# Performance work log

Hardware: AMD Instinct MI355X
Metric: run time of the kernel (lower is better)

## Reference

```python
import jax, jax.numpy as jnp
import numpy as np

NP, NC, E, EL = 50000, 5000, 200000, 100000
DP, DC, HID, OUT, HEADS = 1280, 256, 128, 128, 4


def setup_inputs() -> dict:
    key = jax.random.key(0)
    ks = jax.random.split(key, 40)
    p = lambda k, shp: jax.random.normal(k, shp, dtype=jnp.float32) * 0.05
    inp = {
        "x_protein": jax.random.normal(ks[0], (NP, DP), dtype=jnp.float32),
        "x_class": jax.random.normal(ks[1], (NC, DC), dtype=jnp.float32),
        "src": jax.random.randint(ks[2], (E,), 0, NP),
        "dst": jax.random.randint(ks[3], (E,), 0, NC),
        "edge_label_src": jax.random.randint(ks[4], (EL,), 0, NP),
        "edge_label_dst": jax.random.randint(ks[5], (EL,), 0, NC),
        # SAGEConv, relation protein->class (updates class nodes)
        "sage_pc_Wl": p(ks[6], (DP, HID)), "sage_pc_bl": p(ks[7], (HID,)), "sage_pc_Wr": p(ks[8], (DC, HID)),
        # SAGEConv, relation class->protein (updates protein nodes)
        "sage_cp_Wl": p(ks[9], (DC, HID)), "sage_cp_bl": p(ks[10], (HID,)), "sage_cp_Wr": p(ks[11], (DP, HID)),
        # GATConv p->c (inputs are hidden after conv1)
        "gat_pc_Wsrc": p(ks[12], (HID, HEADS * HID)), "gat_pc_Wdst": p(ks[13], (HID, HEADS * HID)),
        "gat_pc_asrc": p(ks[14], (HEADS, HID)), "gat_pc_adst": p(ks[15], (HEADS, HID)), "gat_pc_b": p(ks[16], (HID,)),
        # GATConv c->p
        "gat_cp_Wsrc": p(ks[17], (HID, HEADS * HID)), "gat_cp_Wdst": p(ks[18], (HID, HEADS * HID)),
        "gat_cp_asrc": p(ks[19], (HEADS, HID)), "gat_cp_adst": p(ks[20], (HEADS, HID)), "gat_cp_b": p(ks[21], (HID,)),
        # final per-node-type Linear (to_hetero duplicates lin per node type)
        "lin_p_W": p(ks[22], (HID, OUT)), "lin_p_b": p(ks[23], (OUT,)),
        "lin_c_W": p(ks[24], (HID, OUT)), "lin_c_b": p(ks[25], (OUT,)),
        # link predictor
        "link_W": p(ks[26], (2 * OUT, 1)), "link_b": p(ks[27], (1,)),
    }
    return inp


def _sage(x_src, x_dst, s, d, Wl, bl, Wr, n_dst):
    # PyG SAGEConv: lin_l(mean_aggr(x_src)) + lin_r(x_dst); lin_l has bias.
    agg = jax.ops.segment_sum(x_src[s], d, num_segments=n_dst)
    cnt = jax.ops.segment_sum(jnp.ones((s.shape[0], 1), x_src.dtype), d, num_segments=n_dst)
    mean = agg / jnp.maximum(cnt, 1.0)
    return mean @ Wl + bl + x_dst @ Wr


def _gat(x_src, x_dst, s, d, Ws, Wd, a_s, a_d, b, n_dst):
    # PyG GATConv bipartite, heads=HEADS, concat=False, add_self_loops=False.
    H, C = a_s.shape
    hs = (x_src @ Ws).reshape(-1, H, C)   # [Ns, H, C]
    hd = (x_dst @ Wd).reshape(-1, H, C)   # [Nd, H, C]
    als = jnp.einsum('nhc,hc->nh', hs, a_s)
    ald = jnp.einsum('nhc,hc->nh', hd, a_d)
    e = jax.nn.leaky_relu(als[s] + ald[d], 0.2)                    # [E, H]
    emax = jax.ops.segment_max(e, d, num_segments=n_dst)          # stable softmax per dst
    ee = jnp.exp(e - emax[d])
    denom = jax.ops.segment_sum(ee, d, num_segments=n_dst)
    alpha = ee / denom[d]                                          # [E, H]
    out = jax.ops.segment_sum(alpha[:, :, None] * hs[s], d, num_segments=n_dst)  # [Nd, H, C]
    return out.mean(axis=1) + b  # concat=False -> mean over heads


def reference(x_protein, x_class, src, dst, edge_label_src, edge_label_dst,
              sage_pc_Wl, sage_pc_bl, sage_pc_Wr,
              sage_cp_Wl, sage_cp_bl, sage_cp_Wr,
              gat_pc_Wsrc, gat_pc_Wdst, gat_pc_asrc, gat_pc_adst, gat_pc_b,
              gat_cp_Wsrc, gat_cp_Wdst, gat_cp_asrc, gat_cp_adst, gat_cp_b,
              lin_p_W, lin_p_b, lin_c_W, lin_c_b, link_W, link_b):
    # Layer 1: hetero SAGE (each node type has exactly one incoming relation)
    h_c = jax.nn.relu(_sage(x_protein, x_class, src, dst, sage_pc_Wl, sage_pc_bl, sage_pc_Wr, NC))
    h_p = jax.nn.relu(_sage(x_class, x_protein, dst, src, sage_cp_Wl, sage_cp_bl, sage_cp_Wr, NP))
    # Layer 2: hetero GAT
    g_c = jax.nn.relu(_gat(h_p, h_c, src, dst, gat_pc_Wsrc, gat_pc_Wdst, gat_pc_asrc, gat_pc_adst, gat_pc_b, NC))
    g_p = jax.nn.relu(_gat(h_c, h_p, dst, src, gat_cp_Wsrc, gat_cp_Wdst, gat_cp_asrc, gat_cp_adst, gat_cp_b, NP))
    # Per-type output projection
    z_p = g_p @ lin_p_W + lin_p_b
    z_c = g_c @ lin_c_W + lin_c_b
    # Link predictor: gather, concat, linear, sigmoid
    ef = jnp.concatenate([z_p[edge_label_src], z_c[edge_label_dst]], axis=-1)  # [EL, 2*OUT]
    return jax.nn.sigmoid(ef @ link_W + link_b).squeeze(-1)
```

## Files before the change

kernel.cpp:

```cpp
#include <hip/hip_runtime.h>
#include <math.h>

#define NPROT 50000
#define NCLS  5000
#define DIMP  1280
#define DIMC  256
#define SCAN_N (NCLS + NPROT)

typedef float4 f4;
typedef __attribute__((ext_vector_type(8))) short short8;
typedef __attribute__((ext_vector_type(4))) float f32x4;

__device__ __forceinline__ unsigned short f2bf(float f){
    unsigned u = __float_as_uint(f);
    u += 0x7FFFu + ((u >> 16) & 1u);
    return (unsigned short)(u >> 16);
}
__device__ __forceinline__ float bf2f(unsigned short b){
    return __uint_as_float(((unsigned)b) << 16);
}
__device__ __forceinline__ void gload_lds16(const void* g, void* l){
    __builtin_amdgcn_global_load_lds((const __attribute__((address_space(1))) void*)g,
                                     (__attribute__((address_space(3))) void*)l, 16, 0, 0);
}

__global__ __launch_bounds__(512) void gemm_p1(const float* __restrict__ Af,
                                               const unsigned short* __restrict__ Bt,
                                               unsigned short* __restrict__ C, int M){
    __shared__ __align__(16) unsigned char As[128*32*4];
    __shared__ __align__(16) unsigned char Bs[256*32*2];
    const int tid  = threadIdx.x;
    const int lane = tid & 63;
    const int w    = tid >> 6;
    const int wm   = w >> 2, wn = w & 3;
    const int row0 = blockIdx.x * 128;
    const int kg = lane >> 4, fr = lane & 15;

    f32x4 acc[4][4] = {};

    for(int k0 = 0; k0 < DIMP; k0 += 32){
        #pragma unroll
        for(int i=0;i<2;i++){
            int c  = i*512 + w*64 + lane;
            int r  = c >> 3, cc = c & 7;
            int scc = cc ^ (r & 7);
            int srow = min(row0 + r, M-1);
            gload_lds16((const void*)(Af + (size_t)srow*DIMP + k0 + scc*4),
                        (void*)(As + (i*512 + w*64)*16));
        }
        #pragma unroll
        for(int i=0;i<2;i++){
            int c  = i*512 + w*64 + lane;
            int r  = c >> 2, cc = c & 3;
            int scc = cc ^ ((r>>1) & 3);
            gload_lds16((const void*)(Bt + (size_t)r*DIMP + k0 + scc*8),
                        (void*)(Bs + (i*512 + w*64)*16));
        }
        __syncthreads();

        short8 aF[4], bF[4];
        #pragma unroll
        for(int m=0;m<4;m++){
            int r = wm*64 + m*16 + fr;
            int b0 = r*128 + kg*32;
            f4 lo = *(const f4*)(As + (( b0      ) ^ ((r&7)<<4)));
            f4 hi = *(const f4*)(As + (( b0 + 16 ) ^ ((r&7)<<4)));
            union { short8 s; unsigned short u[8]; } uu;
            uu.u[0]=f2bf(lo.x); uu.u[1]=f2bf(lo.y); uu.u[2]=f2bf(lo.z); uu.u[3]=f2bf(lo.w);
            uu.u[4]=f2bf(hi.x); uu.u[5]=f2bf(hi.y); uu.u[6]=f2bf(hi.z); uu.u[7]=f2bf(hi.w);
            aF[m] = uu.s;
        }
        #pragma unroll
        for(int n=0;n<4;n++){
            int r = wn*64 + n*16 + fr;
            int b0 = (r*64 + kg*16) ^ (((r>>1)&3)<<4);
            bF[n] = *(const short8*)(Bs + b0);
        }
        #pragma unroll
        for(int m=0;m<4;m++)
        #pragma unroll
        for(int n=0;n<4;n++)
            acc[m][n] = __builtin_amdgcn_mfma_f32_16x16x32_bf16(aF[m], bF[n], acc[m][n], 0, 0, 0);
        __syncthreads();
    }

    #pragma unroll
    for(int m=0;m<4;m++)
    #pragma unroll
    for(int r=0;r<4;r++){
        int row = row0 + wm*64 + m*16 + kg*4 + r;
        if(row < M){
            #pragma unroll
            for(int n=0;n<4;n++)
                C[(size_t)row*256 + wn*64 + n*16 + fr] = f2bf(acc[m][n][r]);
        }
    }
}

#define NPB ((NPROT+127)/128)
#define NCB ((NCLS+127)/128)
__global__ __launch_bounds__(256) void gemm_hs(const unsigned short* __restrict__ Ap,
                                               const unsigned short* __restrict__ Ac,
                                               const unsigned short* __restrict__ Btp,
                                               const unsigned short* __restrict__ Btc,
                                               unsigned short* __restrict__ Cp,
                                               unsigned short* __restrict__ Cc){
    const bool cls = (int)blockIdx.y >= NPB;
    const unsigned short* A  = cls ? Ac : Ap;
    const unsigned short* Bt = cls ? Btc : Btp;
    unsigned short* C = cls ? Cc : Cp;
    const int M = cls ? NCLS : NPROT;
    const int row0 = (cls ? blockIdx.y - NPB : blockIdx.y) * 128;
    const int col0 = blockIdx.x * 128;

    __shared__ __align__(16) unsigned char As[128*32*2];
    __shared__ __align__(16) unsigned char Bs[128*32*2];
    const int tid  = threadIdx.x;
    const int lane = tid & 63;
    const int w    = tid >> 6;
    const int wm   = w >> 1, wn = w & 1;
    const int kg = lane >> 4, fr = lane & 15;

    f32x4 acc[4][4] = {};

    for(int k0 = 0; k0 < 128; k0 += 32){
        #pragma unroll
        for(int i=0;i<2;i++){
            int c  = i*256 + w*64 + lane;
            int r  = c >> 2, cc = c & 3;
            int scc = cc ^ ((r>>1) & 3);
            int srow = min(row0 + r, M-1);
            gload_lds16((const void*)(A + (size_t)srow*128 + k0 + scc*8),
                        (void*)(As + (i*256 + w*64)*16));
        }
        #pragma unroll
        for(int i=0;i<2;i++){
            int c  = i*256 + w*64 + lane;
            int r  = c >> 2, cc = c & 3;
            int scc = cc ^ ((r>>1) & 3);
            gload_lds16((const void*)(Bt + (size_t)(col0 + r)*128 + k0 + scc*8),
                        (void*)(Bs + (i*256 + w*64)*16));
        }
        __syncthreads();

        short8 aF[4], bF[4];
        #pragma unroll
        for(int m=0;m<4;m++){
            int r = wm*64 + m*16 + fr;
            int b0 = (r*64 + kg*16) ^ (((r>>1)&3)<<4);
            aF[m] = *(const short8*)(As + b0);
        }
        #pragma unroll
        for(int n=0;n<4;n++){
            int r = wn*64 + n*16 + fr;
            int b0 = (r*64 + kg*16) ^ (((r>>1)&3)<<4);
            bF[n] = *(const short8*)(Bs + b0);
        }
        #pragma unroll
        for(int m=0;m<4;m++)
        #pragma unroll
        for(int n=0;n<4;n++)
            acc[m][n] = __builtin_amdgcn_mfma_f32_16x16x32_bf16(aF[m], bF[n], acc[m][n], 0, 0, 0);
        __syncthreads();
    }

    #pragma unroll
    for(int m=0;m<4;m++)
    #pragma unroll
    for(int r=0;r<4;r++){
        int row = row0 + wm*64 + m*16 + kg*4 + r;
        if(row < M){
            #pragma unroll
            for(int n=0;n<4;n++)
                C[(size_t)row*512 + col0 + wn*64 + n*16 + fr] = f2bf(acc[m][n][r]);
        }
    }
}

__global__ __launch_bounds__(256) void gemm64(const float* __restrict__ A,
                                              const float* __restrict__ B,
                                              float* __restrict__ C,
                                              int M, int N, int K){
    __shared__ __align__(16) float As[16][68];
    __shared__ __align__(16) float Bs[16][64];
    const int tid = threadIdx.x;
    const int row0 = blockIdx.y * 64;
    const int col0 = blockIdx.x * 64;
    const int ty = tid >> 4;
    const int tx = tid & 15;
    const int m  = tid >> 2;
    const int kq = (tid & 3) << 2;
    const int kb = tid >> 4;
    const int c4 = (tid & 15) << 2;

    float acc[4][4];
#pragma unroll
    for(int i=0;i<4;i++)
#pragma unroll
        for(int j=0;j<4;j++) acc[i][j]=0.f;

    const bool arow_ok = (row0 + m) < M;
    const float* Abase = A + (size_t)(row0 + m) * K + kq;
    const float* Bbase = B + col0 + c4 + (size_t)kb * N;

    for(int k0 = 0; k0 < K; k0 += 16){
        f4 av;
        if(arow_ok) av = *(const f4*)(Abase + k0);
        else        av = make_float4(0.f,0.f,0.f,0.f);
        As[kq+0][m]=av.x; As[kq+1][m]=av.y; As[kq+2][m]=av.z; As[kq+3][m]=av.w;
        *(f4*)&Bs[kb][c4] = *(const f4*)(Bbase + (size_t)k0 * N);
        __syncthreads();
#pragma unroll
        for(int kk=0;kk<16;kk++){
            f4 a = *(const f4*)&As[kk][ty<<2];
            f4 b = *(const f4*)&Bs[kk][tx<<2];
            float ar[4]={a.x,a.y,a.z,a.w};
            float br[4]={b.x,b.y,b.z,b.w};
#pragma unroll
            for(int i=0;i<4;i++)
#pragma unroll
                for(int j=0;j<4;j++) acc[i][j] += ar[i]*br[j];
        }
        __syncthreads();
    }
#pragma unroll
    for(int i=0;i<4;i++){
        int r = row0 + (ty<<2) + i;
        if(r < M){
            f4 v = make_float4(acc[i][0],acc[i][1],acc[i][2],acc[i][3]);
            *(f4*)&C[(size_t)r*N + col0 + (tx<<2)] = v;
        }
    }
}

__global__ __launch_bounds__(256) void gemm_n8_all(const unsigned short* __restrict__ h_p,
                                                   const unsigned short* __restrict__ h_c,
                                                   const float* __restrict__ projP,
                                                   const float* __restrict__ projC,
                                                   float* __restrict__ attP,
                                                   float* __restrict__ attC){
    __shared__ float Bs[2048];
    const int tid = threadIdx.x;
    for(int i=tid;i<1024;i+=256){ Bs[i]=projP[i]; Bs[1024+i]=projC[i]; }
    __syncthreads();
    const int row = blockIdx.x*32 + (tid>>3);
    const int j = tid & 7;
    if(row >= NPROT+NCLS) return;
    const bool cls = row >= NPROT;
    const int r = cls ? row - NPROT : row;
    const unsigned short* a = (cls ? h_c : h_p) + (size_t)r*128;
    const float* B = Bs + (cls ? 1024 : 0);
    float s=0.f;
#pragma unroll
    for(int k=0;k<128;k++) s += bf2f(a[k])*B[k*8+j];
    (cls ? attC : attP)[(size_t)r*8+j]=s;
}

__global__ void prep_weights(const float* __restrict__ Wl_pc, const float* __restrict__ Wr_cp,
                             const float* __restrict__ Wl_cp, const float* __restrict__ Wr_pc,
                             const float* __restrict__ Ws_pc, const float* __restrict__ Ws_cp,
                             unsigned short* __restrict__ BtP, float* __restrict__ WcatC,
                             unsigned short* __restrict__ BtSp, unsigned short* __restrict__ BtSc){
    int t = blockIdx.x*256 + threadIdx.x;
    if(t < 327680){
        int n = t / 1280, k = t % 1280;
        float v = (n<128) ? Wl_pc[(size_t)k*128+n] : Wr_cp[(size_t)k*128+n-128];
        BtP[t] = f2bf(v);
    } else if(t < 393216){
        int i = t - 327680; int k = i>>8, j = i&255;
        WcatC[i] = (j<128) ? Wl_cp[(size_t)k*128+j] : Wr_pc[(size_t)k*128+j-128];
    } else if(t < 458752){
        int i = t - 393216; int n = i>>7, k = i&127;
        BtSp[i] = f2bf(Ws_pc[(size_t)k*512+n]);
    } else {
        int i = t - 458752; int n = i>>7, k = i&127;
        BtSc[i] = f2bf(Ws_cp[(size_t)k*512+n]);
    }
}

__global__ void folds(const float* __restrict__ pcWs, const float* __restrict__ pcAs,
                      const float* __restrict__ pcWd, const float* __restrict__ pcAd,
                      const float* __restrict__ cpWs, const float* __restrict__ cpAs,
                      const float* __restrict__ cpWd, const float* __restrict__ cpAd,
                      const float* __restrict__ lpW, const float* __restrict__ lpb,
                      const float* __restrict__ lcW, const float* __restrict__ lcb,
                      const float* __restrict__ linkW,
                      float* __restrict__ projP, float* __restrict__ projC,
                      float* __restrict__ w_p, float* __restrict__ w_c,
                      float* __restrict__ cpc){
    int blk = blockIdx.x, tid = threadIdx.x;
    if(blk < 8){
        int sec = blk >> 1;
        int t = (blk & 1)*256 + tid;
        const float *W, *a; float* proj; int colbase;
        if(sec==0){ W=pcWs; a=pcAs; proj=projP; colbase=0; }
        else if(sec==1){ W=cpWd; a=cpAd; proj=projP; colbase=4; }
        else if(sec==2){ W=pcWd; a=pcAd; proj=projC; colbase=0; }
        else { W=cpWs; a=cpAs; proj=projC; colbase=4; }
        int k = t >> 2, h = t & 3;
        const float* w = W + (size_t)k*512 + h*128;
        const float* av = a + h*128;
        float s=0.f;
        for(int c=0;c<128;c++) s += w[c]*av[c];
        proj[k*8 + colbase + h] = s;
    } else {
        if(tid < 128){
            float s=0.f;
            for(int o=0;o<128;o++) s += lpW[(size_t)tid*128+o]*linkW[o];
            w_p[tid]=s;
        } else {
            int j=tid-128;
            float s=0.f;
            for(int o=0;o<128;o++) s += lcW[(size_t)j*128+o]*linkW[128+o];
            w_c[j]=s;
        }
        if(tid==0){ float s=0.f; for(int o=0;o<128;o++) s+=lpb[o]*linkW[o];      cpc[0]=s; }
        if(tid==1){ float s=0.f; for(int o=0;o<128;o++) s+=lcb[o]*linkW[128+o];  cpc[1]=s; }
    }
}

__global__ void deg_kernel(const int* __restrict__ src, const int* __restrict__ dst,
                           int* __restrict__ deg, int E){
    int e = blockIdx.x*256 + threadIdx.x;
    if(e>=E) return;
    atomicAdd(&deg[dst[e]],1);
    atomicAdd(&deg[NCLS + src[e]],1);
}

__global__ __launch_bounds__(1024) void scan1(const int* __restrict__ in, int* __restrict__ out,
                                              int* __restrict__ part, int n){
    __shared__ int buf[1024];
    int tid = threadIdx.x;
    int g = blockIdx.x*1024 + tid;
    int v = (g<n) ? in[g] : 0;
    buf[tid] = v;
    __syncthreads();
    for(int o=1;o<1024;o<<=1){
        int t = (tid>=o) ? buf[tid-o] : 0;
        __syncthreads();
        buf[tid] += t;
        __syncthreads();
    }
    if(g<n) out[g] = buf[tid] - v;
    if(tid==1023) part[blockIdx.x] = buf[1023];
}
__global__ __launch_bounds__(64) void scan2(int* __restrict__ part, int nb,
                                            int* __restrict__ out, int n){
    int tid = threadIdx.x;
    int orig = (tid<nb) ? part[tid] : 0;
    int v = orig;
    #pragma unroll
    for(int o=1;o<64;o<<=1){
        int t = __shfl_up(v, o);
        if(tid>=o) v += t;
    }
    if(tid<nb) part[tid] = v - orig;
    if(tid==63) out[n] = v;
}
__global__ __launch_bounds__(1024) void scan3(int* __restrict__ out, const int* __restrict__ part, int n){
    int g = blockIdx.x*1024 + threadIdx.x;
    if(g<n) out[g] += part[blockIdx.x];
}

__global__ void csr_fill(const int* __restrict__ src, const int* __restrict__ dst,
                         const int* __restrict__ off, int* __restrict__ cur,
                         int* __restrict__ adj, int E){
    int e = blockIdx.x*256 + threadIdx.x;
    if(e>=E) return;
    int s = src[e], d = dst[e];
    int pc = atomicAdd(&cur[d],1);        adj[off[d]+pc] = s;
    int pp = atomicAdd(&cur[NCLS+s],1);   adj[off[NCLS+s]+pp] = d;
}

__global__ __launch_bounds__(256) void sage_all(const int* __restrict__ off, const int* __restrict__ adj,
                                                const unsigned short* __restrict__ P1, const float* __restrict__ C1,
                                                const float* __restrict__ bl_pc, const float* __restrict__ bl_cp,
                                                unsigned short* __restrict__ h_c, unsigned short* __restrict__ h_p){
    int v = blockIdx.x*4 + (threadIdx.x>>6);
    int l = threadIdx.x & 63;
    if(v >= SCAN_N) return;
    int b = off[v], deg = off[v+1]-b;
    float a0=0.f, a1=0.f;
    float inv = 1.f/(float)max(deg,1);
    if(v < NCLS){
        for(int i=0;i<deg;i++){
            int s = adj[b+i];
            ushort2 w = *((const ushort2*)P1 + (size_t)s*128 + l);
            a0 += bf2f(w.x); a1 += bf2f(w.y);
        }
        float2 sv = *((const float2*)C1 + (size_t)v*128 + 64 + l);
        float h0 = fmaxf(a0*inv + bl_pc[2*l]   + sv.x, 0.f);
        float h1 = fmaxf(a1*inv + bl_pc[2*l+1] + sv.y, 0.f);
        ushort2 o; o.x=f2bf(h0); o.y=f2bf(h1);
        *((ushort2*)h_c + (size_t)v*64 + l) = o;
    } else {
        int m = v - NCLS;
        for(int i=0;i<deg;i++){
            int d = adj[b+i];
            float2 w = *((const float2*)C1 + (size_t)d*128 + l);
            a0 += w.x; a1 += w.y;
        }
        ushort2 sv = *((const ushort2*)P1 + (size_t)m*128 + 64 + l);
        float h0 = fmaxf(a0*inv + bl_cp[2*l]   + bf2f(sv.x), 0.f);
        float h1 = fmaxf(a1*inv + bl_cp[2*l+1] + bf2f(sv.y), 0.f);
        ushort2 o; o.x=f2bf(h0); o.y=f2bf(h1);
        *((ushort2*)h_p + (size_t)m*64 + l) = o;
    }
}

__global__ __launch_bounds__(128) void gat_all(const int* __restrict__ off, const int* __restrict__ adj,
                                               const float* __restrict__ attP, const float* __restrict__ attC,
                                               const unsigned short* __restrict__ hs_p,
                                               const unsigned short* __restrict__ hs_c,
                                               const float* __restrict__ gb_pc, const float* __restrict__ gb_cp,
                                               const float* __restrict__ w_c, const float* __restrict__ w_p,
                                               const float* __restrict__ cpc,
                                               float* __restrict__ u_c, float* __restrict__ u_p){
    __shared__ float ald[4];
    __shared__ int   adjS[32];
    __shared__ float eeS[32*4];
    __shared__ float red[128];
    __shared__ float den4[4];
    __shared__ float ws2[2];

    int n = blockIdx.x;
    const bool cls = n < NCLS;
    const int node = cls ? n : n - NCLS;
    const float* attS = cls ? attP : attC;
    const float* attD = cls ? attC : attP;
    const int sbase = cls ? 0 : 4;
    const int dbase = cls ? 0 : 4;
    const unsigned short* hs = cls ? hs_p : hs_c;
    const float* gb = cls ? gb_pc : gb_cp;
    const float* wv = cls ? w_c : w_p;
    float* u = cls ? u_c : u_p;
    const int cidx = cls ? 1 : 0;

    int j = threadIdx.x;
    int b = off[n], deg = off[n+1]-b;
    if(j < 4) ald[j] = attD[(size_t)node*8 + dbase + j];

    float acc0=0.f, acc1=0.f, acc2=0.f, acc3=0.f;
    float denP = 0.f;

    for(int base=0; base<deg; base+=32){
        int cnt = min(32, deg-base);
        if(j < cnt) adjS[j] = adj[b+base+j];
        __syncthreads();
        if(j < cnt*4){
            int i = j>>2, h = j&3;
            int s = adjS[i];
            float e = attS[(size_t)s*8 + sbase + h] + ald[h];
            e = e > 0.f ? e : 0.2f*e;
            float ee = __expf(e);
            eeS[j] = ee;
            denP += ee;
        }
        __syncthreads();
        for(int ii=0; ii<cnt; ii++){
            int s = adjS[ii];
            const unsigned short* row = hs + (size_t)s*512;
            float4 ee = *(const float4*)&eeS[ii*4];
            acc0 += ee.x * bf2f(row[j]);
            acc1 += ee.y * bf2f(row[128+j]);
            acc2 += ee.z * bf2f(row[256+j]);
            acc3 += ee.w * bf2f(row[384+j]);
        }
        __syncthreads();
    }

    red[j] = denP;
    __syncthreads();
    if(j < 4){
        float s = 0.f;
        for(int t=j; t<128; t+=4) s += red[t];
        den4[j] = s;
    }
    __syncthreads();

    float outj = 0.f;
    if(deg > 0)
        outj = 0.25f*(acc0/den4[0] + acc1/den4[1] + acc2/den4[2] + acc3/den4[3]);

    float val = fmaxf(outj + gb[j], 0.f) * wv[j];
    #pragma unroll
    for(int o=32;o;o>>=1) val += __shfl_down(val, o);
    if((j & 63) == 0) ws2[j>>6] = val;
    __syncthreads();
    if(j == 0) u[node] = ws2[0] + ws2[1] + cpc[cidx];
}

__global__ void link_out(const int* __restrict__ els, const int* __restrict__ eld,
                         const float* __restrict__ u_p, const float* __restrict__ u_c,
                         const float* __restrict__ linkb, float* __restrict__ out, int EL){
    int i = blockIdx.x*256 + threadIdx.x;
    if(i >= EL) return;
    float x = u_p[els[i]] + u_c[eld[i]] + linkb[0];
    out[i] = 1.f/(1.f + __expf(-x));
}

extern "C" void kernel_launch(void* const* d_in, const int* in_sizes, int n_in,
                              void* d_out, int out_size, void* d_ws, size_t ws_size,
                              hipStream_t stream){
    const float* x_p  = (const float*)d_in[0];
    const float* x_c  = (const float*)d_in[1];
    const int*   src  = (const int*)d_in[2];
    const int*   dst  = (const int*)d_in[3];
    const int*   els  = (const int*)d_in[4];
    const int*   eld  = (const int*)d_in[5];
    const float* sage_pc_Wl = (const float*)d_in[6];
    const float* sage_pc_bl = (const float*)d_in[7];
    const float* sage_pc_Wr = (const float*)d_in[8];
    const float* sage_cp_Wl = (const float*)d_in[9];
    const float* sage_cp_bl = (const float*)d_in[10];
    const float* sage_cp_Wr = (const float*)d_in[11];
    const float* gat_pc_Wsrc = (const float*)d_in[12];
    const float* gat_pc_Wdst = (const float*)d_in[13];
    const float* gat_pc_asrc = (const float*)d_in[14];
    const float* gat_pc_adst = (const float*)d_in[15];
    const float* gat_pc_b    = (const float*)d_in[16];
    const float* gat_cp_Wsrc = (const float*)d_in[17];
    const float* gat_cp_Wdst = (const float*)d_in[18];
    const float* gat_cp_asrc = (const float*)d_in[19];
    const float* gat_cp_adst = (const float*)d_in[20];
    const float* gat_cp_b    = (const float*)d_in[21];
    const float* lin_p_W = (const float*)d_in[22];
    const float* lin_p_b = (const float*)d_in[23];
    const float* lin_c_W = (const float*)d_in[24];
    const float* lin_c_b = (const float*)d_in[25];
    const float* link_W  = (const float*)d_in[26];
    const float* link_b  = (const float*)d_in[27];

    const int E  = in_sizes[2];
    const int EL = in_sizes[4];

    float* ws = (float*)d_ws;
    size_t off = 0;
    auto alloc = [&](size_t n)->float*{ float* p = ws + off; off += (n + 3) & ~(size_t)3; return p; };

    unsigned short* BtP  = (unsigned short*)alloc((size_t)256*DIMP/2);
    float* WcatC = alloc((size_t)DIMC*256);
    unsigned short* BtSp = (unsigned short*)alloc((size_t)512*128/2);
    unsigned short* BtSc = (unsigned short*)alloc((size_t)512*128/2);
    unsigned short* P1   = (unsigned short*)alloc((size_t)NPROT*256/2);
    float* C1    = alloc((size_t)NCLS*256);
    unsigned short* h_p  = (unsigned short*)alloc((size_t)NPROT*128/2);
    unsigned short* h_c  = (unsigned short*)alloc((size_t)NCLS*128/2);
    unsigned short* hs_p = (unsigned short*)alloc((size_t)NPROT*512/2);
    unsigned short* hs_c = (unsigned short*)alloc((size_t)NCLS*512/2);
    float* attP  = alloc((size_t)NPROT*8);
    float* attC  = alloc((size_t)NCLS*8);
    float* projP = alloc(128*8);
    float* projC = alloc(128*8);
    float* w_p   = alloc(128);
    float* w_c   = alloc(128);
    float* cpc   = alloc(4);
    int* degcur = (int*)alloc((size_t)2*SCAN_N);
    int* deg = degcur;
    int* cur = degcur + SCAN_N;
    int* offv = (int*)alloc(SCAN_N+1);
    int* part = (int*)alloc(64);
    int* adj  = (int*)alloc((size_t)2*E);
    float* u_p = alloc(NPROT);
    float* u_c = alloc(NCLS);
    if(off*4 > ws_size) return;

    hipMemsetAsync(degcur, 0, (size_t)2*SCAN_N*4, stream);

    prep_weights<<<2048,256,0,stream>>>(sage_pc_Wl, sage_cp_Wr, sage_cp_Wl, sage_pc_Wr,
                                        gat_pc_Wsrc, gat_cp_Wsrc, BtP, WcatC, BtSp, BtSc);
    folds<<<9,256,0,stream>>>(gat_pc_Wsrc, gat_pc_asrc, gat_pc_Wdst, gat_pc_adst,
                              gat_cp_Wsrc, gat_cp_asrc, gat_cp_Wdst, gat_cp_adst,
                              lin_p_W, lin_p_b, lin_c_W, lin_c_b, link_W,
                              projP, projC, w_p, w_c, cpc);

    deg_kernel<<<(E+255)/256,256,0,stream>>>(src,dst,deg,E);
    const int NB = (SCAN_N + 1023)/1024;
    scan1<<<NB,1024,0,stream>>>(deg, offv, part, SCAN_N);
    scan2<<<1,64,0,stream>>>(part, NB, offv, SCAN_N);
    scan3<<<NB,1024,0,stream>>>(offv, part, SCAN_N);
    csr_fill<<<(E+255)/256,256,0,stream>>>(src,dst,offv,cur,adj,E);

    gemm_p1<<<(NPROT+127)/128,512,0,stream>>>(x_p, BtP, P1, NPROT);
    gemm64<<<dim3(4,(NCLS+63)/64),256,0,stream>>>(x_c, WcatC, C1, NCLS, 256, DIMC);

    sage_all<<<(SCAN_N+3)/4,256,0,stream>>>(offv, adj, P1, C1, sage_pc_bl, sage_cp_bl, h_c, h_p);

    gemm_hs<<<dim3(4,NPB+NCB),256,0,stream>>>(h_p, h_c, BtSp, BtSc, hs_p, hs_c);
    gemm_n8_all<<<(NPROT+NCLS+31)/32,256,0,stream>>>(h_p, h_c, projP, projC, attP, attC);

    gat_all<<<SCAN_N,128,0,stream>>>(offv, adj, attP, attC, hs_p, hs_c,
                                     gat_pc_b, gat_cp_b, w_c, w_p, cpc, u_c, u_p);

    link_out<<<(EL+255)/256,256,0,stream>>>(els, eld, u_p, u_c, link_b, (float*)d_out, EL);
}
```

Before: 360.3 us.

## Fuse setup kernels, drop scan3, fold attention projection into gemm_hs, vectorize GAT gather

Merges weight prep, folds and degree counting into one setup kernel, removes the scan3 pass by adding block partials on read (OFFV), and computes the attention logits inside gemm_hs blocks with blockIdx.x==0 instead of a separate kernel. The GAT aggregation now has each thread load a ushort4 for a single head instead of four scalar loads across heads, then combines heads with a shuffle and an LDS reduction. The aim is fewer launches and better coalesced gathers, at the cost of an extra part[] load on every offset read and uneven work in gemm_hs blocks.

```diff
diff --git a/kernel.cpp b/kernel.cpp
--- a/kernel.cpp
+++ b/kernel.cpp
@@ -22,6 +22,9 @@
 __device__ __forceinline__ void gload_lds16(const void* g, void* l){
     __builtin_amdgcn_global_load_lds((const __attribute__((address_space(1))) void*)g,
                                      (__attribute__((address_space(3))) void*)l, 16, 0, 0);
+}
+__device__ __forceinline__ int OFFV(const int* __restrict__ offv, const int* __restrict__ part, int v){
+    return offv[v] + part[v>>10];
 }
 
 __global__ __launch_bounds__(512) void gemm_p1(const float* __restrict__ Af,
@@ -103,8 +106,12 @@
                                                const unsigned short* __restrict__ Ac,
                                                const unsigned short* __restrict__ Btp,
                                                const unsigned short* __restrict__ Btc,
+                                               const float* __restrict__ projP,
+                                               const float* __restrict__ projC,
                                                unsigned short* __restrict__ Cp,
-                                               unsigned short* __restrict__ Cc){
+                                               unsigned short* __restrict__ Cc,
+                                               float* __restrict__ attP,
+                                               float* __restrict__ attC){
     const bool cls = (int)blockIdx.y >= NPB;
     const unsigned short* A  = cls ? Ac : Ap;
     const unsigned short* Bt = cls ? Btc : Btp;
@@ -115,6 +122,7 @@
 
     __shared__ __align__(16) unsigned char As[128*32*2];
     __shared__ __align__(16) unsigned char Bs[128*32*2];
+    __shared__ float projS[1024];
     const int tid  = threadIdx.x;
     const int lane = tid & 63;
     const int w    = tid >> 6;
@@ -173,6 +181,31 @@
             #pragma unroll
             for(int n=0;n<4;n++)
                 C[(size_t)row*512 + col0 + wn*64 + n*16 + fr] = f2bf(acc[m][n][r]);
+        }
+    }
+
+    if(blockIdx.x == 0){
+        const float* proj = cls ? projC : projP;
+        float* att = cls ? attC : attP;
+        for(int i=tid;i<1024;i+=256) projS[i] = proj[i];
+        __syncthreads();
+        int ri = tid >> 1, cb = (tid & 1)*4;
+        int row = row0 + ri;
+        if(row < M){
+            const unsigned short* ar = A + (size_t)row*128;
+            float s0=0.f,s1=0.f,s2=0.f,s3=0.f;
+            #pragma unroll
+            for(int kk=0;kk<16;kk++){
+                short8 a8 = *(const short8*)(ar + kk*8);
+                #pragma unroll
+                for(int q=0;q<8;q++){
+                    float av = bf2f((unsigned short)a8[q]);
+                    const float* pr = &projS[(kk*8+q)*8 + cb];
+                    s0 += av*pr[0]; s1 += av*pr[1]; s2 += av*pr[2]; s3 += av*pr[3];
+                }
+            }
+            f4 o = make_float4(s0,s1,s2,s3);
+            *(f4*)&att[(size_t)row*8 + cb] = o;
         }
     }
 }
@@ -233,65 +266,42 @@
     }
 }
 
-__global__ __launch_bounds__(256) void gemm_n8_all(const unsigned short* __restrict__ h_p,
-                                                   const unsigned short* __restrict__ h_c,
-                                                   const float* __restrict__ projP,
-                                                   const float* __restrict__ projC,
-                                                   float* __restrict__ attP,
-                                                   float* __restrict__ attC){
-    __shared__ float Bs[2048];
-    const int tid = threadIdx.x;
-    for(int i=tid;i<1024;i+=256){ Bs[i]=projP[i]; Bs[1024+i]=projC[i]; }
-    __syncthreads();
-    const int row = blockIdx.x*32 + (tid>>3);
-    const int j = tid & 7;
-    if(row >= NPROT+NCLS) return;
-    const bool cls = row >= NPROT;
-    const int r = cls ? row - NPROT : row;
-    const unsigned short* a = (cls ? h_c : h_p) + (size_t)r*128;
-    const float* B = Bs + (cls ? 1024 : 0);
-    float s=0.f;
-#pragma unroll
-    for(int k=0;k<128;k++) s += bf2f(a[k])*B[k*8+j];
-    (cls ? attC : attP)[(size_t)r*8+j]=s;
-}
-
-__global__ void prep_weights(const float* __restrict__ Wl_pc, const float* __restrict__ Wr_cp,
-                             const float* __restrict__ Wl_cp, const float* __restrict__ Wr_pc,
-                             const float* __restrict__ Ws_pc, const float* __restrict__ Ws_cp,
-                             unsigned short* __restrict__ BtP, float* __restrict__ WcatC,
-                             unsigned short* __restrict__ BtSp, unsigned short* __restrict__ BtSc){
-    int t = blockIdx.x*256 + threadIdx.x;
-    if(t < 327680){
-        int n = t / 1280, k = t % 1280;
-        float v = (n<128) ? Wl_pc[(size_t)k*128+n] : Wr_cp[(size_t)k*128+n-128];
-        BtP[t] = f2bf(v);
-    } else if(t < 393216){
-        int i = t - 327680; int k = i>>8, j = i&255;
-        WcatC[i] = (j<128) ? Wl_cp[(size_t)k*128+j] : Wr_pc[(size_t)k*128+j-128];
-    } else if(t < 458752){
-        int i = t - 393216; int n = i>>7, k = i&127;
-        BtSp[i] = f2bf(Ws_pc[(size_t)k*512+n]);
-    } else {
-        int i = t - 458752; int n = i>>7, k = i&127;
-        BtSc[i] = f2bf(Ws_cp[(size_t)k*512+n]);
-    }
-}
-
-__global__ void folds(const float* __restrict__ pcWs, const float* __restrict__ pcAs,
+__global__ void setup(const float* __restrict__ Wl_pc, const float* __restrict__ Wr_cp,
+                      const float* __restrict__ Wl_cp, const float* __restrict__ Wr_pc,
+                      const float* __restrict__ pcWs, const float* __restrict__ pcAs,
                       const float* __restrict__ pcWd, const float* __restrict__ pcAd,
                       const float* __restrict__ cpWs, const float* __restrict__ cpAs,
                       const float* __restrict__ cpWd, const float* __restrict__ cpAd,
                       const float* __restrict__ lpW, const float* __restrict__ lpb,
                       const float* __restrict__ lcW, const float* __restrict__ lcb,
                       const float* __restrict__ linkW,
+                      const int* __restrict__ src, const int* __restrict__ dst,
+                      unsigned short* __restrict__ BtP, float* __restrict__ WcatC,
+                      unsigned short* __restrict__ BtSp, unsigned short* __restrict__ BtSc,
                       float* __restrict__ projP, float* __restrict__ projC,
                       float* __restrict__ w_p, float* __restrict__ w_c,
-                      float* __restrict__ cpc){
+                      float* __restrict__ cpc,
+                      int* __restrict__ deg, int E){
     int blk = blockIdx.x, tid = threadIdx.x;
-    if(blk < 8){
-        int sec = blk >> 1;
-        int t = (blk & 1)*256 + tid;
+    if(blk < 2048){
+        int t = blk*256 + tid;
+        if(t < 327680){
+            int n = t / 1280, k = t % 1280;
+            float v = (n<128) ? Wl_pc[(size_t)k*128+n] : Wr_cp[(size_t)k*128+n-128];
+            BtP[t] = f2bf(v);
+        } else if(t < 393216){
+            int i = t - 327680; int k = i>>8, j = i&255;
+            WcatC[i] = (j<128) ? Wl_cp[(size_t)k*128+j] : Wr_pc[(size_t)k*128+j-128];
+        } else if(t < 458752){
+            int i = t - 393216; int n = i>>7, k = i&127;
+            BtSp[i] = f2bf(pcWs[(size_t)k*512+n]);
+        } else {
+            int i = t - 458752; int n = i>>7, k = i&127;
+            BtSc[i] = f2bf(cpWs[(size_t)k*512+n]);
+        }
+    } else if(blk < 2056){
+        int sec = (blk-2048) >> 1;
+        int t = ((blk-2048) & 1)*256 + tid;
         const float *W, *a; float* proj; int colbase;
         if(sec==0){ W=pcWs; a=pcAs; proj=projP; colbase=0; }
         else if(sec==1){ W=cpWd; a=cpAd; proj=projP; colbase=4; }
@@ -303,7 +313,7 @@
         float s=0.f;
         for(int c=0;c<128;c++) s += w[c]*av[c];
         proj[k*8 + colbase + h] = s;
-    } else {
+    } else if(blk == 2056){
         if(tid < 128){
             float s=0.f;
             for(int o=0;o<128;o++) s += lpW[(size_t)tid*128+o]*linkW[o];
@@ -316,15 +326,13 @@
         }
         if(tid==0){ float s=0.f; for(int o=0;o<128;o++) s+=lpb[o]*linkW[o];      cpc[0]=s; }
         if(tid==1){ float s=0.f; for(int o=0;o<128;o++) s+=lcb[o]*linkW[128+o];  cpc[1]=s; }
-    }
-}
-
-__global__ void deg_kernel(const int* __restrict__ src, const int* __restrict__ dst,
-                           int* __restrict__ deg, int E){
-    int e = blockIdx.x*256 + threadIdx.x;
-    if(e>=E) return;
-    atomicAdd(&deg[dst[e]],1);
-    atomicAdd(&deg[NCLS + src[e]],1);
+    } else {
+        int e = (blk-2057)*256 + tid;
+        if(e < E){
+            atomicAdd(&deg[dst[e]],1);
+            atomicAdd(&deg[NCLS + src[e]],1);
+        }
+    }
 }
 
 __global__ __launch_bounds__(1024) void scan1(const int* __restrict__ in, int* __restrict__ out,
@@ -345,7 +353,7 @@
     if(tid==1023) part[blockIdx.x] = buf[1023];
 }
 __global__ __launch_bounds__(64) void scan2(int* __restrict__ part, int nb,
-                                            int* __restrict__ out, int n){
+                                            int* __restrict__ offv, int n){
     int tid = threadIdx.x;
     int orig = (tid<nb) ? part[tid] : 0;
     int v = orig;
@@ -354,32 +362,30 @@
         int t = __shfl_up(v, o);
         if(tid>=o) v += t;
     }
+    int total = __shfl(v, nb-1);
     if(tid<nb) part[tid] = v - orig;
-    if(tid==63) out[n] = v;
-}
-__global__ __launch_bounds__(1024) void scan3(int* __restrict__ out, const int* __restrict__ part, int n){
-    int g = blockIdx.x*1024 + threadIdx.x;
-    if(g<n) out[g] += part[blockIdx.x];
+    if(tid == (n>>10)) offv[n] = total - (v - orig);
 }
 
 __global__ void csr_fill(const int* __restrict__ src, const int* __restrict__ dst,
-                         const int* __restrict__ off, int* __restrict__ cur,
-                         int* __restrict__ adj, int E){
+                         const int* __restrict__ offv, const int* __restrict__ part,
+                         int* __restrict__ cur, int* __restrict__ adj, int E){
     int e = blockIdx.x*256 + threadIdx.x;
     if(e>=E) return;
     int s = src[e], d = dst[e];
-    int pc = atomicAdd(&cur[d],1);        adj[off[d]+pc] = s;
-    int pp = atomicAdd(&cur[NCLS+s],1);   adj[off[NCLS+s]+pp] = d;
-}
-
-__global__ __launch_bounds__(256) void sage_all(const int* __restrict__ off, const int* __restrict__ adj,
+    int pc = atomicAdd(&cur[d],1);        adj[OFFV(offv,part,d)+pc] = s;
+    int pp = atomicAdd(&cur[NCLS+s],1);   adj[OFFV(offv,part,NCLS+s)+pp] = d;
+}
+
+__global__ __launch_bounds__(256) void sage_all(const int* __restrict__ offv, const int* __restrict__ part,
+                                                const int* __restrict__ adj,
                                                 const unsigned short* __restrict__ P1, const float* __restrict__ C1,
                                                 const float* __restrict__ bl_pc, const float* __restrict__ bl_cp,
                                                 unsigned short* __restrict__ h_c, unsigned short* __restrict__ h_p){
     int v = blockIdx.x*4 + (threadIdx.x>>6);
     int l = threadIdx.x & 63;
     if(v >= SCAN_N) return;
-    int b = off[v], deg = off[v+1]-b;
+    int b = OFFV(offv,part,v), deg = OFFV(offv,part,v+1)-b;
     float a0=0.f, a1=0.f;
     float inv = 1.f/(float)max(deg,1);
     if(v < NCLS){
@@ -408,7 +414,8 @@
     }
 }
 
-__global__ __launch_bounds__(128) void gat_all(const int* __restrict__ off, const int* __restrict__ adj,
+__global__ __launch_bounds__(128) void gat_all(const int* __restrict__ offv, const int* __restrict__ part,
+                                               const int* __restrict__ adj,
                                                const float* __restrict__ attP, const float* __restrict__ attC,
                                                const unsigned short* __restrict__ hs_p,
                                                const unsigned short* __restrict__ hs_c,
@@ -421,15 +428,14 @@
     __shared__ float eeS[32*4];
     __shared__ float red[128];
     __shared__ float den4[4];
-    __shared__ float ws2[2];
+    __shared__ f4    red4[32];
 
     int n = blockIdx.x;
     const bool cls = n < NCLS;
     const int node = cls ? n : n - NCLS;
     const float* attS = cls ? attP : attC;
     const float* attD = cls ? attC : attP;
-    const int sbase = cls ? 0 : 4;
-    const int dbase = cls ? 0 : 4;
+    const int abase = cls ? 0 : 4;
     const unsigned short* hs = cls ? hs_p : hs_c;
     const float* gb = cls ? gb_pc : gb_cp;
     const float* wv = cls ? w_c : w_p;
@@ -437,10 +443,12 @@
     const int cidx = cls ? 1 : 0;
 
     int j = threadIdx.x;
-    int b = off[n], deg = off[n+1]-b;
-    if(j < 4) ald[j] = attD[(size_t)node*8 + dbase + j];
-
-    float acc0=0.f, acc1=0.f, acc2=0.f, acc3=0.f;
+    const int hh = j >> 5;
+    const int q  = j & 31;
+    int b = OFFV(offv,part,n), deg = OFFV(offv,part,n+1)-b;
+    if(j < 4) ald[j] = attD[(size_t)node*8 + abase + j];
+
+    float a0=0.f, a1=0.f, a2=0.f, a3=0.f;
     float denP = 0.f;
 
     for(int base=0; base<deg; base+=32){
@@ -450,7 +458,7 @@
         if(j < cnt*4){
             int i = j>>2, h = j&3;
             int s = adjS[i];
-            float e = attS[(size_t)s*8 + sbase + h] + ald[h];
+            float e = attS[(size_t)s*8 + abase + h] + ald[h];
             e = e > 0.f ? e : 0.2f*e;
             float ee = __expf(e);
             eeS[j] = ee;
@@ -459,12 +467,10 @@
         __syncthreads();
         for(int ii=0; ii<cnt; ii++){
             int s = adjS[ii];
-            const unsigned short* row = hs + (size_t)s*512;
-            float4 ee = *(const float4*)&eeS[ii*4];
-            acc0 += ee.x * bf2f(row[j]);
-            acc1 += ee.y * bf2f(row[128+j]);
-            acc2 += ee.z * bf2f(row[256+j]);
-            acc3 += ee.w * bf2f(row[384+j]);
+            float ee = eeS[ii*4 + hh];
+            ushort4 v = *(const ushort4*)(hs + (size_t)s*512 + hh*128 + q*4);
+            a0 += ee*bf2f(v.x); a1 += ee*bf2f(v.y);
+            a2 += ee*bf2f(v.z); a3 += ee*bf2f(v.w);
         }
         __syncthreads();
     }
@@ -478,16 +484,27 @@
     }
     __syncthreads();
 
-    float outj = 0.f;
-    if(deg > 0)
-        outj = 0.25f*(acc0/den4[0] + acc1/den4[1] + acc2/den4[2] + acc3/den4[3]);
-
-    float val = fmaxf(outj + gb[j], 0.f) * wv[j];
+    float inv = (deg > 0) ? 0.25f/den4[hh] : 0.f;
+    a0 *= inv; a1 *= inv; a2 *= inv; a3 *= inv;
+
+    a0 += __shfl_xor(a0, 32); a1 += __shfl_xor(a1, 32);
+    a2 += __shfl_xor(a2, 32); a3 += __shfl_xor(a3, 32);
+    if(j >= 64 && j < 96) red4[q] = make_float4(a0,a1,a2,a3);
+    __syncthreads();
+    float val = 0.f;
+    if(j < 32){
+        f4 r = red4[q];
+        float t0 = a0 + r.x, t1 = a1 + r.y, t2 = a2 + r.z, t3 = a3 + r.w;
+        const float* gbq = gb + q*4;
+        const float* wvq = wv + q*4;
+        val = fmaxf(t0 + gbq[0], 0.f)*wvq[0]
+            + fmaxf(t1 + gbq[1], 0.f)*wvq[1]
+            + fmaxf(t2 + gbq[2], 0.f)*wvq[2]
+            + fmaxf(t3 + gbq[3], 0.f)*wvq[3];
+    }
     #pragma unroll
-    for(int o=32;o;o>>=1) val += __shfl_down(val, o);
-    if((j & 63) == 0) ws2[j>>6] = val;
-    __syncthreads();
-    if(j == 0) u[node] = ws2[0] + ws2[1] + cpc[cidx];
+    for(int o=16;o;o>>=1) val += __shfl_down(val, o);
+    if(j == 0) u[node] = val + cpc[cidx];
 }
 
 __global__ void link_out(const int* __restrict__ els, const int* __restrict__ eld,
@@ -567,29 +584,28 @@
 
     hipMemsetAsync(degcur, 0, (size_t)2*SCAN_N*4, stream);
 
-    prep_weights<<<2048,256,0,stream>>>(sage_pc_Wl, sage_cp_Wr, sage_cp_Wl, sage_pc_Wr,
-                                        gat_pc_Wsrc, gat_cp_Wsrc, BtP, WcatC, BtSp, BtSc);
-    folds<<<9,256,0,stream>>>(gat_pc_Wsrc, gat_pc_asrc, gat_pc_Wdst, gat_pc_adst,
-                              gat_cp_Wsrc, gat_cp_asrc, gat_cp_Wdst, gat_cp_adst,
-                              lin_p_W, lin_p_b, lin_c_W, lin_c_b, link_W,
-                              projP, projC, w_p, w_c, cpc);
-
-    deg_kernel<<<(E+255)/256,256,0,stream>>>(src,dst,deg,E);
+    setup<<<2057 + (E+255)/256, 256, 0, stream>>>(
+        sage_pc_Wl, sage_cp_Wr, sage_cp_Wl, sage_pc_Wr,
+        gat_pc_Wsrc, gat_pc_asrc, gat_pc_Wdst, gat_pc_adst,
+        gat_cp_Wsrc, gat_cp_asrc, gat_cp_Wdst, gat_cp_adst,
+        lin_p_W, lin_p_b, lin_c_W, lin_c_b, link_W,
+        src, dst,
+        BtP, WcatC, BtSp, BtSc, projP, projC, w_p, w_c, cpc, deg, E);
+
     const int NB = (SCAN_N + 1023)/1024;
     scan1<<<NB,1024,0,stream>>>(deg, offv, part, SCAN_N);
     scan2<<<1,64,0,stream>>>(part, NB, offv, SCAN_N);
-    scan3<<<NB,1024,0,stream>>>(offv, part, SCAN_N);
-    csr_fill<<<(E+255)/256,256,0,stream>>>(src,dst,offv,cur,adj,E);
+    csr_fill<<<(E+255)/256,256,0,stream>>>(src,dst,offv,part,cur,adj,E);
 
     gemm_p1<<<(NPROT+127)/128,512,0,stream>>>(x_p, BtP, P1, NPROT);
     gemm64<<<dim3(4,(NCLS+63)/64),256,0,stream>>>(x_c, WcatC, C1, NCLS, 256, DIMC);
 
-    sage_all<<<(SCAN_N+3)/4,256,0,stream>>>(offv, adj, P1, C1, sage_pc_bl, sage_cp_bl, h_c, h_p);
-
-    gemm_hs<<<dim3(4,NPB+NCB),256,0,stream>>>(h_p, h_c, BtSp, BtSc, hs_p, hs_c);
-    gemm_n8_all<<<(NPROT+NCLS+31)/32,256,0,stream>>>(h_p, h_c, projP, projC, attP, attC);
-
-    gat_all<<<SCAN_N,128,0,stream>>>(offv, adj, attP, attC, hs_p, hs_c,
+    sage_all<<<(SCAN_N+3)/4,256,0,stream>>>(offv, part, adj, P1, C1, sage_pc_bl, sage_cp_bl, h_c, h_p);
+
+    gemm_hs<<<dim3(4,NPB+NCB),256,0,stream>>>(h_p, h_c, BtSp, BtSc, projP, projC,
+                                              hs_p, hs_c, attP, attC);
+
+    gat_all<<<SCAN_N,128,0,stream>>>(offv, part, adj, attP, attC, hs_p, hs_c,
                                      gat_pc_b, gat_cp_b, w_c, w_p, cpc, u_c, u_p);
 
     link_out<<<(EL+255)/256,256,0,stream>>>(els, eld, u_p, u_c, link_b, (float*)d_out, EL);
```

Result: no change. 364.9 us (+1.3%).
